# Kernel tuning notes

Hardware: AMD Instinct MI355X
Metric: run time of the kernel (lower is better)

The kernel has to match this reference:

```python
import jax, jax.numpy as jnp
import numpy as np

N_CAT, N_PER = 5, 20
N_NODES = N_CAT * N_PER  # 100
T, IN_DIM, H = 512, 256, 1024


def gru_seq(x, Wih, Whh, bih, bhh):
    # x: (B, T, IN). torch GRU (batch_first), returns all hidden states (B, T, H).
    B = x.shape[0]
    Hd = Whh.shape[1]
    xp = x @ Wih.T + bih  # (B, T, 3H) precomputed input projections

    def step(h, xt):
        gh = h @ Whh.T + bhh
        xr, xz, xn = jnp.split(xt, 3, axis=-1)
        hr, hz, hn = jnp.split(gh, 3, axis=-1)
        r = jax.nn.sigmoid(xr + hr)
        z = jax.nn.sigmoid(xz + hz)
        n = jnp.tanh(xn + r * hn)
        h_new = (1.0 - z) * n + z * h
        return h_new, h_new

    h0 = jnp.zeros((B, Hd), x.dtype)
    _, hs = jax.lax.scan(step, h0, jnp.swapaxes(xp, 0, 1))
    return jnp.swapaxes(hs, 0, 1)  # (B, T, H)


def attention_block(x, Wt, bt):
    # x: (B, T, D). Linear over the time axis, softmax over output-time axis.
    # w[b,u,d] = sum_t x[b,t,d] * Wt[u,t] + bt[u]
    w = jnp.einsum('btd,ut->bud', x, Wt) + bt[None, :, None]
    probs = jax.nn.softmax(w, axis=1)  # softmax over u (time) per (b, d)
    return jnp.sum(probs * x, axis=1)  # (B, D)


def gat_conv(x, edge_index, W, a_src, a_dst, bias):
    # Single-head PyG GATConv with default add_self_loops=True, neg slope 0.2.
    N = x.shape[0]
    loops = jnp.arange(N)
    src = jnp.concatenate([edge_index[0], loops])
    dst = jnp.concatenate([edge_index[1], loops])
    h = x @ W.T  # (N, D)
    alpha_s = h @ a_src  # (N,)
    alpha_d = h @ a_dst
    e = jax.nn.leaky_relu(alpha_s[src] + alpha_d[dst], negative_slope=0.2)
    # segment softmax over incoming edges per target node
    emax = jax.ops.segment_max(e, dst, num_segments=N)
    ex = jnp.exp(e - emax[dst])
    denom = jax.ops.segment_sum(ex, dst, num_segments=N)
    alpha = ex / denom[dst]
    out = jax.ops.segment_sum(alpha[:, None] * h[src], dst, num_segments=N)
    return out + bias


def setup_inputs() -> dict:
    key = jax.random.key(0)
    ks = jax.random.split(key, 24)
    s = 0.05

    def rn(k, shape):
        return jax.random.normal(k, shape, dtype=jnp.float32) * s

    # structured edge lists
    inner = []
    for c in range(N_CAT):
        for i in range(N_PER):
            for j in range(N_PER):
                if i != j:
                    inner.append((c * N_PER + i, c * N_PER + j))
    inner_edge = jnp.asarray(np.array(inner, dtype=np.int64).T)  # (2, 1900)
    outer = [(i, j) for i in range(N_CAT) for j in range(N_CAT) if i != j]
    outer_edge = jnp.asarray(np.array(outer, dtype=np.int64).T)  # (2, 20)

    return {
        'weekly_batch': jax.random.normal(ks[0], (N_NODES, T, IN_DIM), dtype=jnp.float32),
        'gru_Wih': rn(ks[1], (3 * H, IN_DIM)),
        'gru_Whh': rn(ks[2], (3 * H, H)),
        'gru_bih': rn(ks[3], (3 * H,)),
        'gru_bhh': rn(ks[4], (3 * H,)),
        'enc_att_W': rn(ks[5], (T, T)),
        'enc_att_b': rn(ks[6], (T,)),
        'pool_att_W': rn(ks[7], (N_PER, N_PER)),
        'pool_att_b': rn(ks[8], (N_PER,)),
        'inner_W': rn(ks[9], (H, H)),
        'inner_asrc': rn(ks[10], (H,)),
        'inner_adst': rn(ks[11], (H,)),
        'inner_b': rn(ks[12], (H,)),
        'cat_W': rn(ks[13], (H, H)),
        'cat_asrc': rn(ks[14], (H,)),
        'cat_adst': rn(ks[15], (H,)),
        'cat_b': rn(ks[16], (H,)),
        'fusion_W': rn(ks[17], (H, 3 * H)),
        'fusion_b': rn(ks[18], (H,)),
        'reg_W': rn(ks[19], (1, H)),
        'reg_b': rn(ks[20], (1,)),
        'cls_W': rn(ks[21], (1, H)),
        'cls_b': rn(ks[22], (1,)),
        'inner_edge': inner_edge,
        'outer_edge': outer_edge,
    }


def reference(weekly_batch, gru_Wih, gru_Whh, gru_bih, gru_bhh,
              enc_att_W, enc_att_b, pool_att_W, pool_att_b,
              inner_W, inner_asrc, inner_adst, inner_b,
              cat_W, cat_asrc, cat_adst, cat_b,
              fusion_W, fusion_b, reg_W, reg_b, cls_W, cls_b,
              inner_edge, outer_edge):
    # SequenceEncoder: GRU + (eval-mode dropout = identity) + attention pooling
    seq = gru_seq(weekly_batch.reshape(-1, T, IN_DIM), gru_Wih, gru_Whh, gru_bih, gru_bhh)
    v = attention_block(seq, enc_att_W, enc_att_b)  # (100, H)

    # inner GAT over all 100 nodes
    inner_emb = gat_conv(v, inner_edge, inner_W, inner_asrc, inner_adst, inner_b)
    inner_emb = inner_emb.reshape(N_CAT, N_PER, H)
    vv = v.reshape(N_CAT, N_PER, H)

    # pool 20 stocks -> 1 category vector, then category-level GAT
    cat_vec = attention_block(vv, pool_att_W, pool_att_b)  # (5, H)
    cat_vec = gat_conv(cat_vec, outer_edge, cat_W, cat_asrc, cat_adst, cat_b)
    cat_exp = jnp.broadcast_to(cat_vec[:, None, :], (N_CAT, N_PER, H))

    fusion = jnp.concatenate([vv, cat_exp, inner_emb], axis=-1)  # (5, 20, 3H)
    f = jax.nn.relu(fusion @ fusion_W.T + fusion_b)
    reg_out = (f @ reg_W.T + reg_b).reshape(-1)  # (100,)
    cls_out = jax.nn.sigmoid(f @ cls_W.T + cls_b).reshape(-1)  # (100,)
    return reg_out, cls_out
```

## Files before the change

kernel.cpp:

```cpp
#include <hip/hip_runtime.h>
#include <hip/hip_bf16.h>


typedef __bf16 bf16x8 __attribute__((ext_vector_type(8)));
typedef float  floatx4 __attribute__((ext_vector_type(4)));
typedef int    intx4  __attribute__((ext_vector_type(4)));

struct US8 { unsigned short u[8]; };

__device__ __forceinline__ unsigned short f2bf(float f) {
  unsigned u = __builtin_bit_cast(unsigned, f);
  u += 0x7fffu + ((u >> 16) & 1u);
  return (unsigned short)(u >> 16);
}
__device__ __forceinline__ float bf2f(unsigned short h) {
  return __builtin_bit_cast(float, ((unsigned)h) << 16);
}
__device__ __forceinline__ float sigm(float x) { return 1.f / (1.f + __expf(-x)); }

__device__ __forceinline__ void bar_lds() {
  asm volatile("s_waitcnt lgkmcnt(0)" ::: "memory");
  __builtin_amdgcn_s_barrier();
  asm volatile("" ::: "memory");
}

static const size_t OF_XBF   = 0;
static const size_t OF_HIST  = 26214400;
static const size_t OF_ENCW  = 131277824;
static const size_t OF_V     = 131802112;
static const size_t OF_HIN   = 132211712;
static const size_t OF_IEMB  = 132621312;
static const size_t OF_CATV  = 133030912;
static const size_t OF_CATH  = 133051392;
static const size_t OF_CATO  = 133071872;
static const size_t OF_FBUF  = 133092352;
static const size_t OF_FOUT  = 134321152;
static const size_t OF_FLAGS = 134730752;

__global__ void f2bf_kernel(const float* __restrict__ src, unsigned short* __restrict__ dst, int n4) {
  int i = blockIdx.x * 256 + threadIdx.x;
  if (i < n4) {
    float4 v = ((const float4*)src)[i];
    ushort4 o;
    o.x = f2bf(v.x); o.y = f2bf(v.y); o.z = f2bf(v.z); o.w = f2bf(v.w);
    ((ushort4*)dst)[i] = o;
  }
}

#define GRU_LDS 163136
__global__ void __launch_bounds__(320) gru_recur(
    const unsigned short* __restrict__ xbf,
    const float* __restrict__ Whh, const float* __restrict__ Wih,
    const float* __restrict__ bih, const float* __restrict__ bhh,
    unsigned short* hist, int* flags)
{
  extern __shared__ char smem[];
  unsigned* hbf  = (unsigned*)smem;
  unsigned short* Bw  = (unsigned short*)smem;
  float* biasl = (float*)(smem + 122880);
  float* ghp   = (float*)(smem + 123136);
  float* hfp   = (float*)(smem + 161536);

  const int tid  = threadIdx.x;
  const int lane = tid & 63;
  const int w    = tid >> 6;
  const int wg   = blockIdx.x;
  const int g    = wg >> 6;
  const int s    = wg & 63;
  const int gb   = g * 25;
  const int myq  = s >> 4;

  for (int o = tid; o < 7680; o += 320) {
    int kk, ln; const float* sp; unsigned short* dst;
    if (o < 5120) {
      int q = o >= 2560; int rem = o - q * 2560;
      kk = rem >> 6; ln = rem & 63;
      int l = ln & 15, ksub = ln >> 4, j = s * 16 + l;
      int k = kk * 32 + ksub * 8;
      sp = (k < 1024) ? (Whh + (size_t)(q * 1024 + j) * 1024 + k)
                      : (Wih + (size_t)(q * 1024 + j) * 256 + (k - 1024));
      dst = Bw + ((size_t)((q * 40 + kk) * 64 + ln)) * 8;
    } else if (o < 7168) {
      int o2 = o - 5120; kk = o2 >> 6; ln = o2 & 63;
      int l = ln & 15, ksub = ln >> 4, j = s * 16 + l;
      sp = Whh + (size_t)(2048 + j) * 1024 + kk * 32 + ksub * 8;
      dst = Bw + (size_t)(5120 + kk * 64 + ln) * 8;
    } else {
      int o3 = o - 7168; kk = o3 >> 6; ln = o3 & 63;
      int l = ln & 15, ksub = ln >> 4, j = s * 16 + l;
      sp = Wih + (size_t)(2048 + j) * 256 + kk * 32 + ksub * 8;
      dst = Bw + (size_t)(7168 + kk * 64 + ln) * 8;
    }
    float4 f0 = *(const float4*)sp;
    float4 f1 = *(const float4*)(sp + 4);
    dst[0] = f2bf(f0.x); dst[1] = f2bf(f0.y); dst[2] = f2bf(f0.z); dst[3] = f2bf(f0.w);
    dst[4] = f2bf(f1.x); dst[5] = f2bf(f1.y); dst[6] = f2bf(f1.z); dst[7] = f2bf(f1.w);
  }
  if (tid < 16) {
    int j = s * 16 + tid;
    biasl[tid]      = bih[j]        + bhh[j];
    biasl[16 + tid] = bih[1024 + j] + bhh[1024 + j];
    biasl[32 + tid] = bhh[2048 + j];
    biasl[48 + tid] = bih[2048 + j];
  }
  for (int i = tid; i < 400; i += 320) hfp[i] = 0.f;
  __syncthreads();

  bf16x8 Breg[24];
  #pragma unroll
  for (int lk = 0; lk < 8; lk++) {
    int kk = w * 8 + lk;
    Breg[lk * 3 + 0] = __builtin_bit_cast(bf16x8, *(const intx4*)(Bw + (size_t)((kk)      * 64 + lane) * 8));
    Breg[lk * 3 + 1] = __builtin_bit_cast(bf16x8, *(const intx4*)(Bw + (size_t)((40 + kk) * 64 + lane) * 8));
    const unsigned short* np = (w < 4)
        ? (Bw + (size_t)(5120 + kk * 64 + lane) * 8)
        : (Bw + (size_t)(7168 + (kk - 32) * 64 + lane) * 8);
    Breg[lk * 3 + 2] = __builtin_bit_cast(bf16x8, *(const intx4*)np);
  }

  const int kf_x = (lane >> 4) * 8;
  size_t baseA[2], rowx[2];
  #pragma unroll
  for (int mt = 0; mt < 2; mt++) {
    int m = mt * 16 + (lane & 15);
    int bb = (m < 25) ? m : 24;
    baseA[mt] = (size_t)((g * 64 + (lane >> 5)) * 400 + bb * 16 + ((lane >> 4) & 1) * 8);
    rowx[mt]  = (size_t)(gb + bb) * 512 * 256;
  }

  const int* pollline = flags + (wg * 4 + w) * 16;

  for (int t = 0; t < 512; t++) {
    if (w < 4) {
      for (;;) {
        int f = __hip_atomic_load(pollline + (lane & 15), __ATOMIC_RELAXED, __HIP_MEMORY_SCOPE_AGENT);
        if (__all(f >= t)) break;
      }
      asm volatile("" ::: "memory");
    }

    const unsigned short* hrow = hist + (size_t)t * 102400;
    floatx4 acc[2][3];
    #pragma unroll
    for (int mt = 0; mt < 2; mt++)
      #pragma unroll
      for (int gg = 0; gg < 3; gg++) acc[mt][gg] = floatx4{0.f, 0.f, 0.f, 0.f};

    #pragma unroll
    for (int lk = 0; lk < 8; lk++) {
      int kk = w * 8 + lk;
      #pragma unroll
      for (int mt = 0; mt < 2; mt++) {
        const unsigned short* ap = (w < 4)
            ? (hrow + baseA[mt] + (size_t)kk * 800)
            : (xbf + rowx[mt] + (size_t)t * 256 + (kk - 32) * 32 + kf_x);
        bf16x8 a = __builtin_bit_cast(bf16x8, *(const intx4*)ap);
        acc[mt][0] = __builtin_amdgcn_mfma_f32_16x16x32_bf16(a, Breg[lk * 3 + 0], acc[mt][0], 0, 0, 0);
        acc[mt][1] = __builtin_amdgcn_mfma_f32_16x16x32_bf16(a, Breg[lk * 3 + 1], acc[mt][1], 0, 0, 0);
        acc[mt][2] = __builtin_amdgcn_mfma_f32_16x16x32_bf16(a, Breg[lk * 3 + 2], acc[mt][2], 0, 0, 0);
      }
    }

    {
      int base = (lane & 15) * 20 + (lane >> 4) * 4;
      #pragma unroll
      for (int mt = 0; mt < 2; mt++)
        #pragma unroll
        for (int gg = 0; gg < 3; gg++)
          *(floatx4*)(ghp + (size_t)((w * 2 + mt) * 3 + gg) * 320 + base) = acc[mt][gg];
    }
    bar_lds();

    if (tid < 256) {
      int lp = tid >> 5, b = tid & 31;
      if (b < 25) {
        int mt2 = b >> 4, rr = b & 15;
        unsigned packed = 0;
        #pragma unroll
        for (int ii = 0; ii < 2; ii++) {
          int l = lp * 2 + ii;
          int off = l * 20 + rr;
          float ghr = 0.f, ghz = 0.f, ghnh = 0.f, ghnx;
          #pragma unroll
          for (int ww = 0; ww < 4; ww++) {
            const float* gq = ghp + (size_t)((ww * 2 + mt2) * 3) * 320 + off;
            ghr += gq[0]; ghz += gq[320]; ghnh += gq[640];
          }
          { const float* gq = ghp + (size_t)((4 * 2 + mt2) * 3) * 320 + off;
            ghr += gq[0]; ghz += gq[320]; ghnx = gq[640]; }
          float r = sigm(ghr + biasl[l]);
          float z = sigm(ghz + biasl[16 + l]);
          float nv = ghnx + biasl[48 + l] + r * (ghnh + biasl[32 + l]);
          nv = fminf(fmaxf(nv, -15.f), 15.f);
          float e2 = __expf(-2.f * nv);
          float n = (1.f - e2) / (1.f + e2);
          float ho = hfp[l * 25 + b];
          float hn = (1.f - z) * n + z * ho;
          hfp[l * 25 + b] = hn;
          packed |= ((unsigned)f2bf(hn)) << (16 * ii);
        }
        hbf[b * 8 + lp] = packed;
      }
    }
    bar_lds();

    if (w == 4) {
      if (lane < 50) {
        int b = lane >> 1, hs = lane & 1;
        intx4 d = *(const intx4*)&hbf[b * 8 + hs * 4];
        unsigned long long addr = (unsigned long long)(hist + (size_t)(t + 1) * 102400
                                  + (size_t)((g * 64 + s) * 400 + b * 16 + hs * 8));
        asm volatile("global_store_dwordx4 %0, %1, off sc0 sc1" :: "v"(addr), "v"(d) : "memory");
      }
      if (t < 511) {
        asm volatile("s_waitcnt vmcnt(0)" ::: "memory");
        __hip_atomic_store(flags + ((g * 64 + lane) * 4 + myq) * 16 + (s & 15), t + 1,
                           __ATOMIC_RELAXED, __HIP_MEMORY_SCOPE_AGENT);
      }
    }
  }
}

#define ATT_LDS 68096
__global__ void __launch_bounds__(512) att_pool(
    const unsigned short* __restrict__ hist,
    const unsigned short* __restrict__ encw,
    const float* __restrict__ encb,
    float* __restrict__ vout)
{
  extern __shared__ char smem[];
  unsigned short* Bs = (unsigned short*)smem;
  float* red  = (float*)(smem + 65536);
  float* cmax = (float*)(smem + 65536 + 2048);
  float* csum = (float*)(smem + 65536 + 2048 + 256);

  const int tid = threadIdx.x, w = tid >> 6, lane = tid & 63;
  const int q = lane >> 4, col = lane & 15;
  const int n0 = blockIdx.x * 64;
  const int bg = n0 >> 10, d0 = n0 & 1023;
  const int gA = bg / 25, rA = bg - gA * 25;

  for (int ii = 0; ii < 8; ii++) {
    int c = tid + 512 * ii;
    int t = c >> 3, dd = c & 7;
    int sA = (d0 >> 4) + (dd >> 1), hsA = dd & 1;
    intx4 li = *(const intx4*)(hist + (size_t)(t + 1) * 102400
                             + (size_t)((gA * 64 + sA) * 400 + rA * 16 + hsA * 8));
    US8 u8 = __builtin_bit_cast(US8, li);
    int kstep = t >> 5, ksub = (t >> 3) & 3, i = t & 7;
    int ntile = dd >> 1, nc0 = (dd & 1) * 8;
    unsigned short* dst = Bs + ((size_t)((kstep * 4 + ntile) * 64 + ksub * 16 + nc0)) * 8 + i;
    #pragma unroll
    for (int jj = 0; jj < 8; jj++) dst[jj * 8] = u8.u[jj];
  }
  __syncthreads();

  floatx4 acc[4][4];
  #pragma unroll
  for (int mi = 0; mi < 4; mi++)
    #pragma unroll
    for (int ni = 0; ni < 4; ni++) acc[mi][ni] = floatx4{0.f, 0.f, 0.f, 0.f};

  #pragma unroll 2
  for (int kk = 0; kk < 16; kk++) {
    int tch = kk * 32 + q * 8;
    bf16x8 af[4];
    #pragma unroll
    for (int mi = 0; mi < 4; mi++) {
      int u = (w * 4 + mi) * 16 + col;
      af[mi] = __builtin_bit_cast(bf16x8, *(const intx4*)(encw + (size_t)u * 512 + tch));
    }
    #pragma unroll
    for (int ni = 0; ni < 4; ni++) {
      bf16x8 bf = __builtin_bit_cast(bf16x8, *(const intx4*)(Bs + (size_t)((kk * 4 + ni) * 64 + lane) * 8));
      #pragma unroll
      for (int mi = 0; mi < 4; mi++)
        acc[mi][ni] = __builtin_amdgcn_mfma_f32_16x16x32_bf16(af[mi], bf, acc[mi][ni], 0, 0, 0);
    }
  }

  #pragma unroll
  for (int mi = 0; mi < 4; mi++) {
    int ub = (w * 4 + mi) * 16 + q * 4;
    float b0 = encb[ub], b1 = encb[ub + 1], b2 = encb[ub + 2], b3 = encb[ub + 3];
    #pragma unroll
    for (int ni = 0; ni < 4; ni++) {
      acc[mi][ni][0] += b0; acc[mi][ni][1] += b1; acc[mi][ni][2] += b2; acc[mi][ni][3] += b3;
    }
  }
  #pragma unroll
  for (int ni = 0; ni < 4; ni++) {
    float m = -1e30f;
    #pragma unroll
    for (int mi = 0; mi < 4; mi++)
      #pragma unroll
      for (int r = 0; r < 4; r++) m = fmaxf(m, acc[mi][ni][r]);
    m = fmaxf(m, __shfl_xor(m, 16)); m = fmaxf(m, __shfl_xor(m, 32));
    red[w * 64 + ni * 16 + col] = m;
  }
  __syncthreads();
  if (tid < 64) {
    float m = red[tid];
    for (int w2 = 1; w2 < 8; w2++) m = fmaxf(m, red[w2 * 64 + tid]);
    cmax[tid] = m;
  }
  __syncthreads();
  #pragma unroll
  for (int ni = 0; ni < 4; ni++) {
    float cm = cmax[ni * 16 + col];
    float sum = 0.f;
    #pragma unroll
    for (int mi = 0; mi < 4; mi++)
      #pragma unroll
      for (int r = 0; r < 4; r++) {
        float e = __expf(acc[mi][ni][r] - cm);
        acc[mi][ni][r] = e; sum += e;
      }
    sum += __shfl_xor(sum, 16); sum += __shfl_xor(sum, 32);
    red[w * 64 + ni * 16 + col] = sum;
  }
  __syncthreads();
  if (tid < 64) {
    float sm = 0.f;
    for (int w2 = 0; w2 < 8; w2++) sm += red[w2 * 64 + tid];
    csum[tid] = sm;
  }
  __syncthreads();
  #pragma unroll
  for (int ni = 0; ni < 4; ni++) {
    float p = 0.f;
    #pragma unroll
    for (int mi = 0; mi < 4; mi++) {
      int u0 = (w * 4 + mi) * 16 + q * 4;
      int ks = u0 >> 5, ksb = (u0 >> 3) & 3, i0 = u0 & 7;
      const unsigned short* hp = Bs + (size_t)((ks * 4 + ni) * 64 + ksb * 16 + col) * 8 + i0;
      p += acc[mi][ni][0] * bf2f(hp[0]) + acc[mi][ni][1] * bf2f(hp[1])
         + acc[mi][ni][2] * bf2f(hp[2]) + acc[mi][ni][3] * bf2f(hp[3]);
    }
    p += __shfl_xor(p, 16); p += __shfl_xor(p, 32);
    red[w * 64 + ni * 16 + col] = p;
  }
  __syncthreads();
  if (tid < 64) {
    float p = 0.f;
    for (int w2 = 0; w2 < 8; w2++) p += red[w2 * 64 + tid];
    vout[n0 + tid] = p / csum[tid];
  }
}

__global__ void gemm_bt(const float* __restrict__ A, const float* __restrict__ B,
                        float* __restrict__ C, int M, int N, int K,
                        const float* __restrict__ bias, int relu)
{
  __shared__ float Al[16][33];
  __shared__ float Bl[64][33];
  int tx = threadIdx.x;
  int nb = blockIdx.x, mb = blockIdx.y;
  int n = nb * 64 + (tx & 63);
  int mq = tx >> 6;
  float acc[4] = {0.f, 0.f, 0.f, 0.f};
  for (int k0 = 0; k0 < K; k0 += 32) {
    for (int e = tx; e < 512; e += 256) {
      int r = e >> 5, c = e & 31; int m = mb * 16 + r;
      Al[r][c] = (m < M) ? A[(size_t)m * K + k0 + c] : 0.f;
    }
    for (int e = tx; e < 2048; e += 256) {
      int r = e >> 5, c = e & 31;
      Bl[r][c] = B[(size_t)(nb * 64 + r) * K + k0 + c];
    }
    __syncthreads();
    int nn = tx & 63;
    #pragma unroll 8
    for (int c = 0; c < 32; c++) {
      float bv = Bl[nn][c];
      #pragma unroll
      for (int i = 0; i < 4; i++) acc[i] += Al[mq * 4 + i][c] * bv;
    }
    __syncthreads();
  }
  #pragma unroll
  for (int i = 0; i < 4; i++) {
    int m = mb * 16 + mq * 4 + i;
    if (m < M && n < N) {
      float r = acc[i] + (bias ? bias[n] : 0.f);
      if (relu) r = fmaxf(r, 0.f);
      C[(size_t)m * N + n] = r;
    }
  }
}

template <int NN>
__global__ void gat_att(const float* __restrict__ h, const float* __restrict__ asrc,
                        const float* __restrict__ adst, const float* __restrict__ bias,
                        float* __restrict__ out)
{
  __shared__ float asd[2][NN];
  __shared__ float P[NN][NN];
  int c = blockIdx.x, tx = threadIdx.x;
  int wid = tx >> 6, lane = tx & 63;
  for (int idx = wid; idx < 2 * NN; idx += 4) {
    int which = idx >= NN; int j = which ? idx - NN : idx;
    const float* av = which ? adst : asrc;
    float p = 0.f;
    for (int k = lane; k < 1024; k += 64) p += h[(size_t)(c * NN + j) * 1024 + k] * av[k];
    for (int m = 32; m; m >>= 1) p += __shfl_xor(p, m);
    if (lane == 0) asd[which][j] = p;
  }
  __syncthreads();
  if (tx < NN) {
    int i = tx; float mx = -1e30f; float e[NN];
    #pragma unroll
    for (int j = 0; j < NN; j++) {
      float x = asd[0][j] + asd[1][i];
      x = (x < 0.f) ? 0.2f * x : x;
      e[j] = x; mx = fmaxf(mx, x);
    }
    float s = 0.f;
    #pragma unroll
    for (int j = 0; j < NN; j++) { e[j] = __expf(e[j] - mx); s += e[j]; }
    #pragma unroll
    for (int j = 0; j < NN; j++) P[i][j] = e[j] / s;
  }
  __syncthreads();
  for (int ee = tx; ee < NN * 1024; ee += 256) {
    int i = ee >> 10, d = ee & 1023;
    float s = 0.f;
    #pragma unroll
    for (int j = 0; j < NN; j++) s += P[i][j] * h[(size_t)(c * NN + j) * 1024 + d];
    out[(size_t)(c * NN + i) * 1024 + d] = s + bias[d];
  }
}

__global__ void pool_att(const float* __restrict__ v, const float* __restrict__ pW,
                         const float* __restrict__ pb, float* __restrict__ catv)
{
  __shared__ float W[400]; __shared__ float bsh[20];
  int tx = threadIdx.x;
  for (int i = tx; i < 400; i += 256) W[i] = pW[i];
  if (tx < 20) bsh[tx] = pb[tx];
  __syncthreads();
  int gid = blockIdx.x * 256 + tx;
  int c = gid >> 10, d = gid & 1023;
  float vals[20];
  #pragma unroll
  for (int t = 0; t < 20; t++) vals[t] = v[(size_t)(c * 20 + t) * 1024 + d];
  float wv[20]; float mx = -1e30f;
  #pragma unroll
  for (int u = 0; u < 20; u++) {
    float s = bsh[u];
    #pragma unroll
    for (int t = 0; t < 20; t++) s += vals[t] * W[u * 20 + t];
    wv[u] = s; mx = fmaxf(mx, s);
  }
  float sum = 0.f, out = 0.f;
  #pragma unroll
  for (int u = 0; u < 20; u++) { float e = __expf(wv[u] - mx); sum += e; out += e * vals[u]; }
  catv[gid] = out / sum;
}

__global__ void concat_kernel(const float* __restrict__ v, const float* __restrict__ cato,
                              const float* __restrict__ iemb, float* __restrict__ F)
{
  int gid = blockIdx.x * 256 + threadIdx.x;
  if (gid < 307200) {
    int i = gid / 3072;
    int k = gid - i * 3072;
    float r;
    if (k < 1024)       r = v[(size_t)i * 1024 + k];
    else if (k < 2048)  r = cato[(size_t)(i / 20) * 1024 + (k - 1024)];
    else                r = iemb[(size_t)i * 1024 + (k - 2048)];
    F[gid] = r;
  }
}

__global__ void heads(const float* __restrict__ f, const float* __restrict__ rw,
                      const float* __restrict__ rb, const float* __restrict__ cw,
                      const float* __restrict__ cb, float* __restrict__ out)
{
  int b = blockIdx.x * 4 + (threadIdx.x >> 6);
  int lane = threadIdx.x & 63;
  float pr = 0.f, pc = 0.f;
  for (int k = lane; k < 1024; k += 64) {
    float x = f[(size_t)b * 1024 + k];
    pr += x * rw[k]; pc += x * cw[k];
  }
  for (int m = 32; m; m >>= 1) { pr += __shfl_xor(pr, m); pc += __shfl_xor(pc, m); }
  if (lane == 0) {
    out[b] = pr + rb[0];
    out[100 + b] = sigm(pc + cb[0]);
  }
}

extern "C" void kernel_launch(void* const* d_in, const int* in_sizes, int n_in,
                              void* d_out, int out_size, void* d_ws, size_t ws_size,
                              hipStream_t stream)
{
  const float* x     = (const float*)d_in[0];
  const float* Wih   = (const float*)d_in[1];
  const float* Whh   = (const float*)d_in[2];
  const float* bih   = (const float*)d_in[3];
  const float* bhh   = (const float*)d_in[4];
  const float* encW  = (const float*)d_in[5];
  const float* encb  = (const float*)d_in[6];
  const float* poolW = (const float*)d_in[7];
  const float* poolb = (const float*)d_in[8];
  const float* innW  = (const float*)d_in[9];
  const float* innas = (const float*)d_in[10];
  const float* innad = (const float*)d_in[11];
  const float* innb  = (const float*)d_in[12];
  const float* catW  = (const float*)d_in[13];
  const float* catas = (const float*)d_in[14];
  const float* catad = (const float*)d_in[15];
  const float* catb  = (const float*)d_in[16];
  const float* fusW  = (const float*)d_in[17];
  const float* fusb  = (const float*)d_in[18];
  const float* regW  = (const float*)d_in[19];
  const float* regb  = (const float*)d_in[20];
  const float* clsW  = (const float*)d_in[21];
  const float* clsb  = (const float*)d_in[22];
  float* out = (float*)d_out;
  char* ws = (char*)d_ws;

  unsigned short* xbf  = (unsigned short*)(ws + OF_XBF);
  unsigned short* hist = (unsigned short*)(ws + OF_HIST);
  int*            flg  = (int*)(ws + OF_FLAGS);
  unsigned short* ewbf = (unsigned short*)(ws + OF_ENCW);
  float* v    = (float*)(ws + OF_V);
  float* hin  = (float*)(ws + OF_HIN);
  float* iemb = (float*)(ws + OF_IEMB);
  float* catv = (float*)(ws + OF_CATV);
  float* cath = (float*)(ws + OF_CATH);
  float* cato = (float*)(ws + OF_CATO);
  float* fbuf = (float*)(ws + OF_FBUF);
  float* fout = (float*)(ws + OF_FOUT);

  (void)hipFuncSetAttribute((const void*)gru_recur, hipFuncAttributeMaxDynamicSharedMemorySize, GRU_LDS);
  (void)hipFuncSetAttribute((const void*)att_pool,  hipFuncAttributeMaxDynamicSharedMemorySize, ATT_LDS);

  (void)hipMemsetAsync(hist, 0, 204800, stream);
  (void)hipMemsetAsync(flg, 0, 65536, stream);

  f2bf_kernel<<<12800, 256, 0, stream>>>(x, xbf, 13107200 / 4);
  f2bf_kernel<<<256,   256, 0, stream>>>(encW, ewbf, 262144 / 4);

  gru_recur<<<256, 320, GRU_LDS, stream>>>(xbf, Whh, Wih, bih, bhh, hist, flg);
  att_pool<<<1600, 512, ATT_LDS, stream>>>(hist, ewbf, encb, v);

  gemm_bt<<<dim3(16, 7), 256, 0, stream>>>(v, innW, hin, 100, 1024, 1024, nullptr, 0);
  gat_att<20><<<5, 256, 0, stream>>>(hin, innas, innad, innb, iemb);
  pool_att<<<20, 256, 0, stream>>>(v, poolW, poolb, catv);
  gemm_bt<<<dim3(16, 1), 256, 0, stream>>>(catv, catW, cath, 5, 1024, 1024, nullptr, 0);
  gat_att<5><<<1, 256, 0, stream>>>(cath, catas, catad, catb, cato);
  concat_kernel<<<1200, 256, 0, stream>>>(v, cato, iemb, fbuf);
  gemm_bt<<<dim3(16, 7), 256, 0, stream>>>(fbuf, fusW, fout, 100, 1024, 3072, fusb, 1);
  heads<<<25, 256, 0, stream>>>(fout, regW, regb, clsW, clsb, out);

  (void)in_sizes; (void)n_in; (void)out_size; (void)ws_size;
}
```

Before: 4.219 ms.

## Run GRU recurrence on 64 workgroups each covering all 100 sequences

Before, the persistent GRU kernel used 256 workgroups: 4 groups of 25 sequences, each split across 64 column slices, with per-step flag synchronisation inside each group. Now 64 workgroups each process all 100 batch rows (7 M-tiles) for their 16 hidden columns. This cuts the number of communicating workgroups and flag traffic per step, and the hidden state now stays in registers with a vectorised epilogue. In exchange each step does more MFMA and global-load work per workgroup on fewer CUs, which could lengthen the serial critical path.

```diff
diff --git a/kernel.cpp b/kernel.cpp
--- a/kernel.cpp
+++ b/kernel.cpp
@@ -47,27 +47,57 @@
   }
 }
 
-#define GRU_LDS 163136
-__global__ void __launch_bounds__(320) gru_recur(
+__device__ __forceinline__ void gru_epi(int u, floatx4& h4, const float* ghp,
+                                        const float* biasl, unsigned short* hb16) {
+  int l = u & 15, q = u >> 4;
+  int mt2 = q >> 2, rr0 = (q & 3) * 4;
+  const float* g0 = ghp + (size_t)(mt2 * 3) * 320 + l * 20 + rr0;
+  floatx4 ghr  = *(const floatx4*)(g0);
+  floatx4 ghz  = *(const floatx4*)(g0 + 320);
+  floatx4 ghnh = *(const floatx4*)(g0 + 640);
+  #pragma unroll
+  for (int ww = 1; ww < 4; ww++) {
+    const float* gq = g0 + ww * (21 * 320);
+    ghr  += *(const floatx4*)(gq);
+    ghz  += *(const floatx4*)(gq + 320);
+    ghnh += *(const floatx4*)(gq + 640);
+  }
+  const float* gx = g0 + 4 * (21 * 320);
+  ghr += *(const floatx4*)(gx);
+  ghz += *(const floatx4*)(gx + 320);
+  floatx4 ghnx = *(const floatx4*)(gx + 640);
+  float br = biasl[l], bz = biasl[16 + l], bnh = biasl[32 + l], bnx = biasl[48 + l];
+  #pragma unroll
+  for (int j = 0; j < 4; j++) {
+    float r = sigm(ghr[j] + br);
+    float z = sigm(ghz[j] + bz);
+    float nv = ghnx[j] + bnx + r * (ghnh[j] + bnh);
+    nv = fminf(fmaxf(nv, -15.f), 15.f);
+    float e2 = __expf(-2.f * nv);
+    float n = (1.f - e2) / (1.f + e2);
+    float hn = (1.f - z) * n + z * h4[j];
+    h4[j] = hn;
+    hb16[(q * 4 + j) * 16 + l] = f2bf(hn);
+  }
+}
+
+#define GRU_LDS 137856
+__global__ void __launch_bounds__(320, 2) gru_recur(
     const unsigned short* __restrict__ xbf,
     const float* __restrict__ Whh, const float* __restrict__ Wih,
     const float* __restrict__ bih, const float* __restrict__ bhh,
     unsigned short* hist, int* flags)
 {
   extern __shared__ char smem[];
-  unsigned* hbf  = (unsigned*)smem;
+  float* ghp  = (float*)smem;
+  unsigned short* hb16 = (unsigned short*)(smem + 134400);
+  float* biasl = (float*)(smem + 137600);
   unsigned short* Bw  = (unsigned short*)smem;
-  float* biasl = (float*)(smem + 122880);
-  float* ghp   = (float*)(smem + 123136);
-  float* hfp   = (float*)(smem + 161536);
 
   const int tid  = threadIdx.x;
   const int lane = tid & 63;
   const int w    = tid >> 6;
-  const int wg   = blockIdx.x;
-  const int g    = wg >> 6;
-  const int s    = wg & 63;
-  const int gb   = g * 25;
+  const int s    = blockIdx.x;
   const int myq  = s >> 4;
 
   for (int o = tid; o < 7680; o += 320) {
@@ -103,7 +133,6 @@
     biasl[32 + tid] = bhh[2048 + j];
     biasl[48 + tid] = bih[2048 + j];
   }
-  for (int i = tid; i < 400; i += 320) hfp[i] = 0.f;
   __syncthreads();
 
   bf16x8 Breg[24];
@@ -117,18 +146,22 @@
         : (Bw + (size_t)(7168 + (kk - 32) * 64 + lane) * 8);
     Breg[lk * 3 + 2] = __builtin_bit_cast(bf16x8, *(const intx4*)np);
   }
-
+  __syncthreads();
+
+  const int kf_h = ((lane >> 4) & 1) * 8;
   const int kf_x = (lane >> 4) * 8;
-  size_t baseA[2], rowx[2];
-  #pragma unroll
-  for (int mt = 0; mt < 2; mt++) {
+  int baseA[7], rowx[7];
+  #pragma unroll
+  for (int mt = 0; mt < 7; mt++) {
     int m = mt * 16 + (lane & 15);
-    int bb = (m < 25) ? m : 24;
-    baseA[mt] = (size_t)((g * 64 + (lane >> 5)) * 400 + bb * 16 + ((lane >> 4) & 1) * 8);
-    rowx[mt]  = (size_t)(gb + bb) * 512 * 256;
-  }
-
-  const int* pollline = flags + (wg * 4 + w) * 16;
+    int bb = (m < 100) ? m : 99;
+    baseA[mt] = (lane >> 5) * 1600 + bb * 16 + kf_h;
+    rowx[mt]  = bb * 131072;
+  }
+
+  const int* pollline = flags + (s * 4 + w) * 16;
+  floatx4 h4a = {0.f, 0.f, 0.f, 0.f};
+  floatx4 h4b = {0.f, 0.f, 0.f, 0.f};
 
   for (int t = 0; t < 512; t++) {
     if (w < 4) {
@@ -140,9 +173,10 @@
     }
 
     const unsigned short* hrow = hist + (size_t)t * 102400;
-    floatx4 acc[2][3];
-    #pragma unroll
-    for (int mt = 0; mt < 2; mt++)
+    const unsigned short* xrow = xbf + t * 256;
+    floatx4 acc[7][3];
+    #pragma unroll
+    for (int mt = 0; mt < 7; mt++)
       #pragma unroll
       for (int gg = 0; gg < 3; gg++) acc[mt][gg] = floatx4{0.f, 0.f, 0.f, 0.f};
 
@@ -150,10 +184,10 @@
     for (int lk = 0; lk < 8; lk++) {
       int kk = w * 8 + lk;
       #pragma unroll
-      for (int mt = 0; mt < 2; mt++) {
+      for (int mt = 0; mt < 7; mt++) {
         const unsigned short* ap = (w < 4)
-            ? (hrow + baseA[mt] + (size_t)kk * 800)
-            : (xbf + rowx[mt] + (size_t)t * 256 + (kk - 32) * 32 + kf_x);
+            ? (hrow + baseA[mt] + kk * 3200)
+            : (xrow + rowx[mt] + (kk - 32) * 32 + kf_x);
         bf16x8 a = __builtin_bit_cast(bf16x8, *(const intx4*)ap);
         acc[mt][0] = __builtin_amdgcn_mfma_f32_16x16x32_bf16(a, Breg[lk * 3 + 0], acc[mt][0], 0, 0, 0);
         acc[mt][1] = __builtin_amdgcn_mfma_f32_16x16x32_bf16(a, Breg[lk * 3 + 1], acc[mt][1], 0, 0, 0);
@@ -162,59 +196,39 @@
     }
 
     {
-      int base = (lane & 15) * 20 + (lane >> 4) * 4;
-      #pragma unroll
-      for (int mt = 0; mt < 2; mt++)
+      int pb = (lane & 15) * 20 + (lane >> 4) * 4;
+      #pragma unroll
+      for (int mt = 0; mt < 7; mt++)
         #pragma unroll
         for (int gg = 0; gg < 3; gg++)
-          *(floatx4*)(ghp + (size_t)((w * 2 + mt) * 3 + gg) * 320 + base) = acc[mt][gg];
+          *(floatx4*)(ghp + (size_t)((w * 7 + mt) * 3 + gg) * 320 + pb) = acc[mt][gg];
     }
     bar_lds();
 
-    if (tid < 256) {
-      int lp = tid >> 5, b = tid & 31;
-      if (b < 25) {
-        int mt2 = b >> 4, rr = b & 15;
-        unsigned packed = 0;
-        #pragma unroll
-        for (int ii = 0; ii < 2; ii++) {
-          int l = lp * 2 + ii;
-          int off = l * 20 + rr;
-          float ghr = 0.f, ghz = 0.f, ghnh = 0.f, ghnx;
-          #pragma unroll
-          for (int ww = 0; ww < 4; ww++) {
-            const float* gq = ghp + (size_t)((ww * 2 + mt2) * 3) * 320 + off;
-            ghr += gq[0]; ghz += gq[320]; ghnh += gq[640];
-          }
-          { const float* gq = ghp + (size_t)((4 * 2 + mt2) * 3) * 320 + off;
-            ghr += gq[0]; ghz += gq[320]; ghnx = gq[640]; }
-          float r = sigm(ghr + biasl[l]);
-          float z = sigm(ghz + biasl[16 + l]);
-          float nv = ghnx + biasl[48 + l] + r * (ghnh + biasl[32 + l]);
-          nv = fminf(fmaxf(nv, -15.f), 15.f);
-          float e2 = __expf(-2.f * nv);
-          float n = (1.f - e2) / (1.f + e2);
-          float ho = hfp[l * 25 + b];
-          float hn = (1.f - z) * n + z * ho;
-          hfp[l * 25 + b] = hn;
-          packed |= ((unsigned)f2bf(hn)) << (16 * ii);
-        }
-        hbf[b * 8 + lp] = packed;
+    gru_epi(tid, h4a, ghp, biasl, hb16);
+    if (tid < 80) gru_epi(tid + 320, h4b, ghp, biasl, hb16);
+
+    bar_lds();
+
+    if (w == 4) {
+      unsigned long long hbase = (unsigned long long)(hist + (size_t)(t + 1) * 102400
+                                                      + (size_t)s * 1600);
+      #pragma unroll
+      for (int i = 0; i < 3; i++) {
+        int c = lane + 64 * i;
+        intx4 d = *(const intx4*)(hb16 + c * 8);
+        asm volatile("global_store_dwordx4 %0, %1, off sc0 sc1"
+                     :: "v"(hbase + (unsigned long long)c * 16), "v"(d) : "memory");
       }
-    }
-    bar_lds();
-
-    if (w == 4) {
-      if (lane < 50) {
-        int b = lane >> 1, hs = lane & 1;
-        intx4 d = *(const intx4*)&hbf[b * 8 + hs * 4];
-        unsigned long long addr = (unsigned long long)(hist + (size_t)(t + 1) * 102400
-                                  + (size_t)((g * 64 + s) * 400 + b * 16 + hs * 8));
-        asm volatile("global_store_dwordx4 %0, %1, off sc0 sc1" :: "v"(addr), "v"(d) : "memory");
+      if (lane < 8) {
+        int c = 192 + lane;
+        intx4 d = *(const intx4*)(hb16 + c * 8);
+        asm volatile("global_store_dwordx4 %0, %1, off sc0 sc1"
+                     :: "v"(hbase + (unsigned long long)c * 16), "v"(d) : "memory");
       }
       if (t < 511) {
         asm volatile("s_waitcnt vmcnt(0)" ::: "memory");
-        __hip_atomic_store(flags + ((g * 64 + lane) * 4 + myq) * 16 + (s & 15), t + 1,
+        __hip_atomic_store(flags + (lane * 4 + myq) * 16 + (s & 15), t + 1,
                            __ATOMIC_RELAXED, __HIP_MEMORY_SCOPE_AGENT);
       }
     }
@@ -237,15 +251,14 @@
   const int tid = threadIdx.x, w = tid >> 6, lane = tid & 63;
   const int q = lane >> 4, col = lane & 15;
   const int n0 = blockIdx.x * 64;
-  const int bg = n0 >> 10, d0 = n0 & 1023;
-  const int gA = bg / 25, rA = bg - gA * 25;
+  const int bA = n0 >> 10, d0 = n0 & 1023;
 
   for (int ii = 0; ii < 8; ii++) {
     int c = tid + 512 * ii;
     int t = c >> 3, dd = c & 7;
     int sA = (d0 >> 4) + (dd >> 1), hsA = dd & 1;
     intx4 li = *(const intx4*)(hist + (size_t)(t + 1) * 102400
-                             + (size_t)((gA * 64 + sA) * 400 + rA * 16 + hsA * 8));
+                             + (size_t)(sA * 1600 + bA * 16 + hsA * 8));
     US8 u8 = __builtin_bit_cast(US8, li);
     int kstep = t >> 5, ksub = (t >> 3) & 3, i = t & 7;
     int ntile = dd >> 1, nc0 = (dd & 1) * 8;
@@ -543,7 +556,7 @@
   f2bf_kernel<<<12800, 256, 0, stream>>>(x, xbf, 13107200 / 4);
   f2bf_kernel<<<256,   256, 0, stream>>>(encW, ewbf, 262144 / 4);
 
-  gru_recur<<<256, 320, GRU_LDS, stream>>>(xbf, Whh, Wih, bih, bhh, hist, flg);
+  gru_recur<<<64, 320, GRU_LDS, stream>>>(xbf, Whh, Wih, bih, bhh, hist, flg);
   att_pool<<<1600, 512, ATT_LDS, stream>>>(hist, ewbf, encb, v);
 
   gemm_bt<<<dim3(16, 7), 256, 0, stream>>>(v, innW, hin, 100, 1024, 1024, nullptr, 0);
```

Result: slower. 12.21 ms (+189.3%).

## Split GAT into score and aggregation kernels, fuse concat into fusion GEMM, pipeline flag polls

Applied to the files above, without the earlier changes.

The GAT attention kernel is split into a small kernel that computes the softmax scores and a separate aggregation kernel launched with many blocks. Before, aggregation ran on only 5 blocks (or 1 for the category GAT). The concat kernel and its buffer are removed, and the fusion GEMM now gathers directly from v, cato and iemb. The GRU flag spin loop now keeps three loads in flight before the check, to cut polling latency. The trade-offs are extra launches and a polling scheme that tests a value up to three loads old, which could add an iteration of wait.

```diff
diff --git a/kernel.cpp b/kernel.cpp
--- a/kernel.cpp
+++ b/kernel.cpp
@@ -132,9 +132,14 @@
 
   for (int t = 0; t < 512; t++) {
     if (w < 4) {
+      const int* fp = pollline + (lane & 15);
+      int f0 = __hip_atomic_load(fp, __ATOMIC_RELAXED, __HIP_MEMORY_SCOPE_AGENT);
+      int f1 = __hip_atomic_load(fp, __ATOMIC_RELAXED, __HIP_MEMORY_SCOPE_AGENT);
+      int f2 = __hip_atomic_load(fp, __ATOMIC_RELAXED, __HIP_MEMORY_SCOPE_AGENT);
       for (;;) {
-        int f = __hip_atomic_load(pollline + (lane & 15), __ATOMIC_RELAXED, __HIP_MEMORY_SCOPE_AGENT);
-        if (__all(f >= t)) break;
+        int f3 = __hip_atomic_load(fp, __ATOMIC_RELAXED, __HIP_MEMORY_SCOPE_AGENT);
+        if (__all(f0 >= t)) break;
+        f0 = f1; f1 = f2; f2 = f3;
       }
       asm volatile("" ::: "memory");
     }
@@ -389,13 +394,58 @@
   }
 }
 
+__global__ void gemm_fuse(const float* __restrict__ v, const float* __restrict__ cato,
+                          const float* __restrict__ iemb, const float* __restrict__ B,
+                          float* __restrict__ C, const float* __restrict__ bias)
+{
+  __shared__ float Al[16][33];
+  __shared__ float Bl[64][33];
+  int tx = threadIdx.x;
+  int nb = blockIdx.x, mb = blockIdx.y;
+  int n = nb * 64 + (tx & 63);
+  int mq = tx >> 6;
+  float acc[4] = {0.f, 0.f, 0.f, 0.f};
+  for (int k0 = 0; k0 < 3072; k0 += 32) {
+    for (int e = tx; e < 512; e += 256) {
+      int r = e >> 5, c = e & 31; int m = mb * 16 + r;
+      float aval = 0.f;
+      if (m < 100) {
+        int k = k0 + c;
+        if (k < 1024)       aval = v[(size_t)m * 1024 + k];
+        else if (k < 2048)  aval = cato[(size_t)(m / 20) * 1024 + (k - 1024)];
+        else                aval = iemb[(size_t)m * 1024 + (k - 2048)];
+      }
+      Al[r][c] = aval;
+    }
+    for (int e = tx; e < 2048; e += 256) {
+      int r = e >> 5, c = e & 31;
+      Bl[r][c] = B[(size_t)(nb * 64 + r) * 3072 + k0 + c];
+    }
+    __syncthreads();
+    int nn = tx & 63;
+    #pragma unroll 8
+    for (int c = 0; c < 32; c++) {
+      float bv = Bl[nn][c];
+      #pragma unroll
+      for (int i = 0; i < 4; i++) acc[i] += Al[mq * 4 + i][c] * bv;
+    }
+    __syncthreads();
+  }
+  #pragma unroll
+  for (int i = 0; i < 4; i++) {
+    int m = mb * 16 + mq * 4 + i;
+    if (m < 100) {
+      float r = fmaxf(acc[i] + bias[n], 0.f);
+      C[(size_t)m * 1024 + n] = r;
+    }
+  }
+}
+
 template <int NN>
-__global__ void gat_att(const float* __restrict__ h, const float* __restrict__ asrc,
-                        const float* __restrict__ adst, const float* __restrict__ bias,
-                        float* __restrict__ out)
+__global__ void gat_scores(const float* __restrict__ h, const float* __restrict__ asrc,
+                           const float* __restrict__ adst, float* __restrict__ P)
 {
   __shared__ float asd[2][NN];
-  __shared__ float P[NN][NN];
   int c = blockIdx.x, tx = threadIdx.x;
   int wid = tx >> 6, lane = tx & 63;
   for (int idx = wid; idx < 2 * NN; idx += 4) {
@@ -419,16 +469,22 @@
     #pragma unroll
     for (int j = 0; j < NN; j++) { e[j] = __expf(e[j] - mx); s += e[j]; }
     #pragma unroll
-    for (int j = 0; j < NN; j++) P[i][j] = e[j] / s;
-  }
-  __syncthreads();
-  for (int ee = tx; ee < NN * 1024; ee += 256) {
-    int i = ee >> 10, d = ee & 1023;
-    float s = 0.f;
-    #pragma unroll
-    for (int j = 0; j < NN; j++) s += P[i][j] * h[(size_t)(c * NN + j) * 1024 + d];
-    out[(size_t)(c * NN + i) * 1024 + d] = s + bias[d];
-  }
+    for (int j = 0; j < NN; j++) P[(size_t)(c * NN + i) * NN + j] = e[j] / s;
+  }
+}
+
+template <int NN>
+__global__ void gat_agg(const float* __restrict__ h, const float* __restrict__ P,
+                        const float* __restrict__ bias, float* __restrict__ out)
+{
+  int gid = blockIdx.x * 256 + threadIdx.x;
+  int i = gid >> 10, d = gid & 1023;
+  int c = i / NN, il = i - c * NN;
+  float s = 0.f;
+  #pragma unroll
+  for (int j = 0; j < NN; j++)
+    s += P[(size_t)(c * NN + il) * NN + j] * h[(size_t)(c * NN + j) * 1024 + d];
+  out[(size_t)i * 1024 + d] = s + bias[d];
 }
 
 __global__ void pool_att(const float* __restrict__ v, const float* __restrict__ pW,
@@ -456,21 +512,6 @@
   #pragma unroll
   for (int u = 0; u < 20; u++) { float e = __expf(wv[u] - mx); sum += e; out += e * vals[u]; }
   catv[gid] = out / sum;
-}
-
-__global__ void concat_kernel(const float* __restrict__ v, const float* __restrict__ cato,
-                              const float* __restrict__ iemb, float* __restrict__ F)
-{
-  int gid = blockIdx.x * 256 + threadIdx.x;
-  if (gid < 307200) {
-    int i = gid / 3072;
-    int k = gid - i * 3072;
-    float r;
-    if (k < 1024)       r = v[(size_t)i * 1024 + k];
-    else if (k < 2048)  r = cato[(size_t)(i / 20) * 1024 + (k - 1024)];
-    else                r = iemb[(size_t)i * 1024 + (k - 2048)];
-    F[gid] = r;
-  }
 }
 
 __global__ void heads(const float* __restrict__ f, const float* __restrict__ rw,
@@ -531,7 +572,8 @@
   float* catv = (float*)(ws + OF_CATV);
   float* cath = (float*)(ws + OF_CATH);
   float* cato = (float*)(ws + OF_CATO);
-  float* fbuf = (float*)(ws + OF_FBUF);
+  float* P20  = (float*)(ws + OF_FBUF);
+  float* P5   = (float*)(ws + OF_FBUF + 16384);
   float* fout = (float*)(ws + OF_FOUT);
 
   (void)hipFuncSetAttribute((const void*)gru_recur, hipFuncAttributeMaxDynamicSharedMemorySize, GRU_LDS);
@@ -547,12 +589,13 @@
   att_pool<<<1600, 512, ATT_LDS, stream>>>(hist, ewbf, encb, v);
 
   gemm_bt<<<dim3(16, 7), 256, 0, stream>>>(v, innW, hin, 100, 1024, 1024, nullptr, 0);
-  gat_att<20><<<5, 256, 0, stream>>>(hin, innas, innad, innb, iemb);
+  gat_scores<20><<<5, 256, 0, stream>>>(hin, innas, innad, P20);
+  gat_agg<20><<<400, 256, 0, stream>>>(hin, P20, innb, iemb);
   pool_att<<<20, 256, 0, stream>>>(v, poolW, poolb, catv);
   gemm_bt<<<dim3(16, 1), 256, 0, stream>>>(catv, catW, cath, 5, 1024, 1024, nullptr, 0);
-  gat_att<5><<<1, 256, 0, stream>>>(cath, catas, catad, catb, cato);
-  concat_kernel<<<1200, 256, 0, stream>>>(v, cato, iemb, fbuf);
-  gemm_bt<<<dim3(16, 7), 256, 0, stream>>>(fbuf, fusW, fout, 100, 1024, 3072, fusb, 1);
+  gat_scores<5><<<1, 256, 0, stream>>>(cath, catas, catad, P5);
+  gat_agg<5><<<20, 256, 0, stream>>>(cath, P5, catb, cato);
+  gemm_fuse<<<dim3(16, 7), 256, 0, stream>>>(v, cato, iemb, fusW, fout, fusb);
   heads<<<25, 256, 0, stream>>>(fout, regW, regb, clsW, clsb, out);
 
   (void)in_sizes; (void)n_in; (void)out_size; (void)ws_size;
```

After: 4.401 ms. +4.3%, slower.
